# Kernel optimization log

Measured on AMD Instinct MI355X. Metric: run time of the kernel, lower is better.

Reference implementation:

```python
import jax, jax.numpy as jnp
import numpy as np

EMBED = 1024
HEADS = 16
HEAD_DIM = EMBED // HEADS
B, S = 4, 2048


def setup_inputs() -> dict:
    key = jax.random.key(0)
    ks = jax.random.split(key, 13)
    std = 1.0 / np.sqrt(EMBED)
    inp = {
        "q": jax.random.normal(ks[0], (B, S, EMBED), jnp.float32),
        "k": jax.random.normal(ks[1], (B, S, EMBED), jnp.float32),
        "v": jax.random.normal(ks[2], (B, S, EMBED), jnp.float32),
        "mask": jax.random.randint(ks[3], (B, 1, S, S), 0, 2, jnp.int32),
        "wq_w": jax.random.normal(ks[4], (EMBED, EMBED), jnp.float32) * std,
        "wq_b": jax.random.normal(ks[5], (EMBED,), jnp.float32) * std,
        "wk_w": jax.random.normal(ks[6], (EMBED, EMBED), jnp.float32) * std,
        "wk_b": jax.random.normal(ks[7], (EMBED,), jnp.float32) * std,
        "wv_w": jax.random.normal(ks[8], (EMBED, EMBED), jnp.float32) * std,
        "wv_b": jax.random.normal(ks[9], (EMBED,), jnp.float32) * std,
        "fo_w": jax.random.normal(ks[10], (EMBED, EMBED), jnp.float32) * std,
        "fo_b": jax.random.normal(ks[11], (EMBED,), jnp.float32) * std,
    }
    return inp


def reference(q, k, v, mask, wq_w, wq_b, wk_w, wk_b, wv_w, wv_b, fo_w, fo_b):
    N = q.shape[0]
    # linear projections (torch Linear: x @ W.T + b)
    qp = (q @ wq_w.T + wq_b).reshape(N, -1, HEADS, HEAD_DIM)
    kp = (k @ wk_w.T + wk_b).reshape(N, -1, HEADS, HEAD_DIM)
    vp = (v @ wv_w.T + wv_b).reshape(N, -1, HEADS, HEAD_DIM)
    # [N, H, Q, K] scores
    energy = jnp.einsum('nqhd,nkhd->nhqk', qp, kp)
    energy = jnp.where(mask == 0, jnp.float32(-1e20), energy)
    # NOTE: original scales by sqrt(embed_size), not sqrt(head_dim)
    attention = jax.nn.softmax(energy / np.float32(np.sqrt(EMBED)), axis=3)
    out = jnp.einsum('nhql,nlhd->nqhd', attention, vp).reshape(N, -1, EMBED)
    return out @ fo_w.T + fo_b
```

## Files before the change

kernel.cpp:

```cpp
#include <hip/hip_runtime.h>

typedef __attribute__((ext_vector_type(4))) float f32x4;
typedef __attribute__((ext_vector_type(16))) float f32x16;
typedef __attribute__((ext_vector_type(8))) __bf16 bf16x8;
typedef __attribute__((ext_vector_type(8))) unsigned short ushort8;
typedef __attribute__((ext_vector_type(4))) unsigned short ushort4v;
typedef __attribute__((ext_vector_type(4))) unsigned uint4v;

#define EMBED 1024
#define SEQ   2048
#define BATCH 4
#define HEADS 16
#define HDIM  64
#define SCL 0.045084220027780106f

#define GLD_LDS16(g, l) __builtin_amdgcn_global_load_lds( \
    (const __attribute__((address_space(1))) void*)(g),   \
    (__attribute__((address_space(3))) void*)(l), 16, 0, 0)
#define GLD_LDS4(g, l) __builtin_amdgcn_global_load_lds(  \
    (const __attribute__((address_space(1))) void*)(g),   \
    (__attribute__((address_space(3))) void*)(l), 4, 0, 0)

static __device__ __forceinline__ unsigned short f2bf(float f) {
  unsigned u = __builtin_bit_cast(unsigned, f);
  u += 0x7FFFu + ((u >> 16) & 1u);
  return (unsigned short)(u >> 16);
}
static __device__ __forceinline__ unsigned cvtpk(float a, float b) {
  unsigned r;
  asm("v_cvt_pk_bf16_f32 %0, %1, %2" : "=v"(r) : "v"(a), "v"(b));
  return r;
}

__global__ __launch_bounds__(256) void pack_mask_kernel(
    const int* __restrict__ m, unsigned long long* __restrict__ out) {
  int t = blockIdx.x * 256 + threadIdx.x;
  unsigned long long bits = __ballot(m[t] != 0);
  if ((threadIdx.x & 63) == 0) out[t >> 6] = bits;
}

__global__ __launch_bounds__(256) void cvt_kernel(
    const float* __restrict__ s, unsigned short* __restrict__ d, int nvec) {
  int i = blockIdx.x * 256 + threadIdx.x;
  if (i >= nvec) return;
  f32x4 a = ((const f32x4*)s)[2 * i];
  f32x4 b = ((const f32x4*)s)[2 * i + 1];
  ushort8 o;
#pragma unroll
  for (int j = 0; j < 4; ++j) { o[j] = f2bf(a[j]); o[4 + j] = f2bf(b[j]); }
  ((ushort8*)d)[i] = o;
}

__global__ __launch_bounds__(256) void cvt4_kernel(
    const float* __restrict__ s0, const float* __restrict__ s1,
    const float* __restrict__ s2, const float* __restrict__ s3,
    unsigned short* __restrict__ d, int nvec) {
  int i = blockIdx.x * 256 + threadIdx.x;
  if (i >= nvec) return;
  const float* s = (blockIdx.y == 0) ? s0 : (blockIdx.y == 1) ? s1
                 : (blockIdx.y == 2) ? s2 : s3;
  unsigned short* dd = d + (size_t)blockIdx.y * nvec * 8;
  f32x4 a = ((const f32x4*)s)[2 * i];
  f32x4 b = ((const f32x4*)s)[2 * i + 1];
  ushort8 o;
#pragma unroll
  for (int j = 0; j < 4; ++j) { o[j] = f2bf(a[j]); o[4 + j] = f2bf(b[j]); }
  ((ushort8*)dd)[i] = o;
}

template<int OUT_MODE>
__global__ __launch_bounds__(256, 3) void gemm_bt(
    const unsigned short* __restrict__ A, const unsigned short* __restrict__ B,
    const float* __restrict__ bias, void* __restrict__ outp) {
  __shared__ unsigned short Ab[3 * 128 * 32];
  __shared__ unsigned short Bb[3 * 128 * 32];
  const int tid = threadIdx.x, lane = tid & 63, wv = tid >> 6;
  const int wy = wv >> 1, wx = wv & 1, ln = lane & 15, g = lane >> 4;
  const int mbase = blockIdx.x * 128, nbase = blockIdx.y * 128;

  const int srow = tid >> 2, scol = (tid & 3) * 16;
  const char* Ag = (const char*)(A + (size_t)(mbase + srow) * EMBED) + scol;
  const char* Bg = (const char*)(B + (size_t)(nbase + srow) * EMBED) + scol;
  const size_t R64 = (size_t)64 * EMBED * 2;

  f32x4 acc[4][4];
#pragma unroll
  for (int i = 0; i < 4; i++)
#pragma unroll
    for (int j = 0; j < 4; j++) acc[i][j] = (f32x4){0.f, 0.f, 0.f, 0.f};

  auto STAGE = [&](int buf, int kt) {
    const size_t koff = (size_t)kt * 64;
    char* al = (char*)Ab + buf * 8192 + tid * 16;
    char* bl = (char*)Bb + buf * 8192 + tid * 16;
    GLD_LDS16(Ag + koff, al);
    GLD_LDS16(Ag + koff + R64, al + 4096);
    GLD_LDS16(Bg + koff, bl);
    GLD_LDS16(Bg + koff + R64, bl + 4096);
  };

  STAGE(0, 0);
  STAGE(1, 1);
  const int NT = EMBED / 32;
  int buf = 0;
  for (int kt = 0; kt < NT; ++kt) {
    __builtin_amdgcn_s_barrier();
    if (kt + 2 < NT) {
      int nb = buf + 2; if (nb >= 3) nb -= 3;
      STAGE(nb, kt + 2);
      asm volatile("s_waitcnt vmcnt(8)" ::: "memory");
    } else if (kt + 1 < NT) {
      asm volatile("s_waitcnt vmcnt(4)" ::: "memory");
    } else {
      asm volatile("s_waitcnt vmcnt(0)" ::: "memory");
    }
    __builtin_amdgcn_sched_barrier(0);
    bf16x8 af[4], bfr[4];
#pragma unroll
    for (int ms = 0; ms < 4; ++ms)
      af[ms] = __builtin_bit_cast(bf16x8,
          *(const ushort8*)&Ab[buf * 4096 + (wy * 64 + ms * 16 + ln) * 32 + g * 8]);
#pragma unroll
    for (int ns = 0; ns < 4; ++ns)
      bfr[ns] = __builtin_bit_cast(bf16x8,
          *(const ushort8*)&Bb[buf * 4096 + (wx * 64 + ns * 16 + ln) * 32 + g * 8]);
#pragma unroll
    for (int ms = 0; ms < 4; ++ms)
#pragma unroll
      for (int ns = 0; ns < 4; ++ns)
        acc[ms][ns] = __builtin_amdgcn_mfma_f32_16x16x32_bf16(
            af[ms], bfr[ns], acc[ms][ns], 0, 0, 0);
    buf = (buf == 2) ? 0 : buf + 1;
  }

  float bv[4];
#pragma unroll
  for (int ns = 0; ns < 4; ++ns) bv[ns] = bias[nbase + wx * 64 + ns * 16 + ln];

  if (OUT_MODE == 0) {
    unsigned short* out = (unsigned short*)outp;
#pragma unroll
    for (int ms = 0; ms < 4; ++ms)
#pragma unroll
      for (int ns = 0; ns < 4; ++ns) {
        int col = nbase + wx * 64 + ns * 16 + ln;
#pragma unroll
        for (int j = 0; j < 4; ++j) {
          int row = mbase + wy * 64 + ms * 16 + g * 4 + j;
          out[(size_t)row * EMBED + col] = f2bf(acc[ms][ns][j] + bv[ns]);
        }
      }
  } else if (OUT_MODE == 1) {
    unsigned short* out = (unsigned short*)outp;
#pragma unroll
    for (int ms = 0; ms < 4; ++ms)
#pragma unroll
      for (int ns = 0; ns < 4; ++ns) {
        int row0 = mbase + wy * 64 + ms * 16 + g * 4;
        int col = nbase + wx * 64 + ns * 16 + ln;
        int b = row0 >> 11, s0 = row0 & (SEQ - 1);
        int h = col >> 6, d = col & 63;
        ushort4v pk;
#pragma unroll
        for (int j = 0; j < 4; ++j) pk[j] = f2bf(acc[ms][ns][j] + bv[ns]);
        *(ushort4v*)&out[(size_t)((b * HEADS + h) * HDIM + d) * SEQ + s0] = pk;
      }
  } else {
    float* out = (float*)outp;
#pragma unroll
    for (int ms = 0; ms < 4; ++ms)
#pragma unroll
      for (int ns = 0; ns < 4; ++ns) {
        int col = nbase + wx * 64 + ns * 16 + ln;
#pragma unroll
        for (int j = 0; j < 4; ++j) {
          int row = mbase + wy * 64 + ms * 16 + g * 4 + j;
          out[(size_t)row * EMBED + col] = acc[ms][ns][j] + bv[ns];
        }
      }
  }
}

__global__ __launch_bounds__(512, 4) void attn5_kernel(
    const unsigned short* __restrict__ qp, const unsigned short* __restrict__ kp,
    const unsigned short* __restrict__ vpT,
    const unsigned long long* __restrict__ mask64,
    unsigned short* __restrict__ attb) {
  __shared__ unsigned char lds[55296];
  unsigned char* Kb = lds;
  unsigned char* Vb = lds + 24576;
  unsigned char* Mb = lds + 49152;

  const int tid = threadIdx.x;
  const int lane = tid & 63, wv = tid >> 6;
  const int lo = lane & 31, hi = lane >> 5;

  const int flat = blockIdx.x + 8 * blockIdx.y + 128 * blockIdx.z;
  const int bh = (flat & 7) * 8 + ((flat >> 3) & 7);
  const int qc = flat >> 6;
  const int b = bh >> 4, h = bh & 15;
  const int qb = qc * 256 + wv * 32;
  const int q = qb + lo;

  bf16x8 qf[4];
  {
    const unsigned short* qr = qp + (size_t)(b * SEQ + q) * EMBED + h * HDIM + hi * 8;
#pragma unroll
    for (int c = 0; c < 4; ++c) {
      ushort8 u = *(const ushort8*)(qr + 16 * c);
      bf16x8 f;
#pragma unroll
      for (int j = 0; j < 8; ++j) {
        float x = __builtin_bit_cast(float, (unsigned)u[j] << 16) * SCL;
        f[j] = (__bf16)x;
      }
      qf[c] = f;
    }
  }

  const int srow = tid >> 3;
  const int srcc = ((tid & 7) * 16) ^ (((tid >> 3) & 7) << 4);
  const char* kbase = (const char*)kp
      + ((size_t)(b * SEQ + srow) * EMBED + h * HDIM) * 2 + srcc;
  const char* vbase = (const char*)vpT
      + ((size_t)((b * HEADS + h) * HDIM + srow)) * SEQ * 2 + srcc;
  const char* mgbase = (const char*)mask64
      + ((size_t)(b * SEQ + qc * 256 + (tid >> 1)) * 32) * 8 + (tid & 1) * 4;

  auto STAGE = [&](int buf, int kt) {
    GLD_LDS16(kbase + (size_t)kt * 64 * EMBED * 2, Kb + buf * 8192 + tid * 16);
    GLD_LDS16(vbase + (size_t)kt * 128, Vb + buf * 8192 + tid * 16);
    GLD_LDS4(mgbase + kt * 8, Mb + buf * 2048 + tid * 4);
  };

  f32x16 oacc0, oacc1, oacc2;
#pragma unroll
  for (int i = 0; i < 16; ++i) { oacc0[i] = 0.f; oacc1[i] = 0.f; oacc2[i] = 0.f; }
  bf16x8 ones;
#pragma unroll
  for (int j = 0; j < 8; ++j) ones[j] = (__bf16)1.0f;

  const int swz = (lo & 7) << 4;

  STAGE(0, 0);
  STAGE(1, 1);
  const int NT = SEQ / 64;
  int buf = 0;
  for (int kt = 0; kt < NT; ++kt) {
    __builtin_amdgcn_s_barrier();
    if (kt + 2 < NT) {
      int nb = buf + 2; if (nb >= 3) nb -= 3;
      STAGE(nb, kt + 2);
      asm volatile("s_waitcnt vmcnt(6)" ::: "memory");
    } else if (kt + 1 < NT) {
      asm volatile("s_waitcnt vmcnt(3)" ::: "memory");
    } else {
      asm volatile("s_waitcnt vmcnt(0)" ::: "memory");
    }
    __builtin_amdgcn_sched_barrier(0);
    const unsigned char* Kc = Kb + buf * 8192;
    const unsigned char* Vc = Vb + buf * 8192;
    const unsigned long long mw =
        *(const unsigned long long*)(Mb + buf * 2048 + (wv * 32 + lo) * 8);

    bf16x8 PA[4];
#pragma unroll
    for (int kg = 0; kg < 2; ++kg) {
      f32x16 e;
#pragma unroll
      for (int i = 0; i < 16; ++i) e[i] = 0.f;
      const int krow = kg * 32 + lo;
#pragma unroll
      for (int c = 0; c < 4; ++c) {
        const int colb = (16 * c + 8 * hi) * 2;
        bf16x8 kf = *(const bf16x8*)(Kc + krow * 128 + (colb ^ swz));
        e = __builtin_amdgcn_mfma_f32_32x32x16_bf16(kf, qf[c], e, 0, 0, 0);
      }
      const unsigned mh = (unsigned)(mw >> (kg * 32 + 4 * hi));
      float p[16];
#pragma unroll
      for (int m = 0; m < 4; ++m)
#pragma unroll
        for (int j = 0; j < 4; ++j) {
          float pe = __builtin_amdgcn_exp2f(e[4 * m + j]);
          p[4 * m + j] = (mh & (1u << (8 * m + j))) ? pe : 0.f;
        }
      unsigned wA0 = cvtpk(p[0], p[1]),   wB0 = cvtpk(p[2], p[3]);
      unsigned wA1 = cvtpk(p[4], p[5]),   wB1 = cvtpk(p[6], p[7]);
      unsigned wA2 = cvtpk(p[8], p[9]),   wB2 = cvtpk(p[10], p[11]);
      unsigned wA3 = cvtpk(p[12], p[13]), wB3 = cvtpk(p[14], p[15]);
      asm("v_permlane32_swap_b32 %0, %1" : "+v"(wA0), "+v"(wA1));
      asm("v_permlane32_swap_b32 %0, %1" : "+v"(wB0), "+v"(wB1));
      asm("v_permlane32_swap_b32 %0, %1" : "+v"(wA2), "+v"(wA3));
      asm("v_permlane32_swap_b32 %0, %1" : "+v"(wB2), "+v"(wB3));
      PA[2 * kg]     = __builtin_bit_cast(bf16x8, (uint4v){wA0, wB0, wA1, wB1});
      PA[2 * kg + 1] = __builtin_bit_cast(bf16x8, (uint4v){wA2, wB2, wA3, wB3});
    }

    __builtin_amdgcn_s_setprio(1);
#pragma unroll
    for (int c = 0; c < 4; ++c) {
      const int pcolb = 32 * c + 16 * hi;
      bf16x8 pf = PA[c];
      {
        bf16x8 vf = *(const bf16x8*)(Vc + lo * 128 + (pcolb ^ swz));
        oacc0 = __builtin_amdgcn_mfma_f32_32x32x16_bf16(pf, vf, oacc0, 0, 0, 0);
      }
      {
        const int drow = 32 + lo;
        bf16x8 vf = *(const bf16x8*)(Vc + drow * 128 + (pcolb ^ swz));
        oacc1 = __builtin_amdgcn_mfma_f32_32x32x16_bf16(pf, vf, oacc1, 0, 0, 0);
      }
      oacc2 = __builtin_amdgcn_mfma_f32_32x32x16_bf16(pf, ones, oacc2, 0, 0, 0);
    }
    __builtin_amdgcn_s_setprio(0);
    buf = (buf == 2) ? 0 : buf + 1;
  }

#pragma unroll
  for (int r = 0; r < 16; ++r) {
    const int qq = qb + (r & 3) + 8 * (r >> 2) + 4 * hi;
    const float dinv = 1.0f / oacc2[r];
    unsigned short* orow = attb + (size_t)(b * SEQ + qq) * EMBED + h * HDIM;
    orow[lo] = f2bf(oacc0[r] * dinv);
    orow[32 + lo] = f2bf(oacc1[r] * dinv);
  }
}

extern "C" void kernel_launch(void* const* d_in, const int* in_sizes, int n_in,
                              void* d_out, int out_size, void* d_ws, size_t ws_size,
                              hipStream_t stream) {
  const float* q    = (const float*)d_in[0];
  const float* k    = (const float*)d_in[1];
  const float* v    = (const float*)d_in[2];
  const int*   mask = (const int*)d_in[3];
  const float* wq_w = (const float*)d_in[4];
  const float* wq_b = (const float*)d_in[5];
  const float* wk_w = (const float*)d_in[6];
  const float* wk_b = (const float*)d_in[7];
  const float* wv_w = (const float*)d_in[8];
  const float* wv_b = (const float*)d_in[9];
  const float* fo_w = (const float*)d_in[10];
  const float* fo_b = (const float*)d_in[11];

  char* ws = (char*)d_ws;
  const size_t MB = 1024 * 1024;
  unsigned short* stage = (unsigned short*)(ws);
  unsigned short* wqb   = (unsigned short*)(ws + 16 * MB);
  unsigned short* qp    = (unsigned short*)(ws + 24 * MB);
  unsigned short* kp    = (unsigned short*)(ws + 40 * MB);
  unsigned short* vpT   = (unsigned short*)(ws + 56 * MB);
  unsigned long long* m64 = (unsigned long long*)(ws + 72 * MB);

  const int NVX = BATCH * SEQ * EMBED / 8;
  const int NVW = EMBED * EMBED / 8;

  pack_mask_kernel<<<(BATCH * SEQ * SEQ) / 256, 256, 0, stream>>>(mask, m64);

  cvt4_kernel<<<dim3(NVW / 256, 4), 256, 0, stream>>>(wq_w, wk_w, wv_w, fo_w, wqb, NVW);
  unsigned short* wkb = wqb + (size_t)NVW * 8;
  unsigned short* wvb = wkb + (size_t)NVW * 8;
  unsigned short* fob = wvb + (size_t)NVW * 8;

  dim3 gg((BATCH * SEQ) / 128, EMBED / 128);
  cvt_kernel<<<NVX / 256, 256, 0, stream>>>(q, stage, NVX);
  gemm_bt<0><<<gg, 256, 0, stream>>>(stage, wqb, wq_b, qp);
  cvt_kernel<<<NVX / 256, 256, 0, stream>>>(k, stage, NVX);
  gemm_bt<0><<<gg, 256, 0, stream>>>(stage, wkb, wk_b, kp);
  cvt_kernel<<<NVX / 256, 256, 0, stream>>>(v, stage, NVX);
  gemm_bt<1><<<gg, 256, 0, stream>>>(stage, wvb, wv_b, vpT);

  attn5_kernel<<<dim3(8, HEADS, BATCH), 512, 0, stream>>>(qp, kp, vpT, m64, stage);

  gemm_bt<2><<<gg, 256, 0, stream>>>(stage, fob, fo_b, (float*)d_out);
}
```

Baseline: 260.8 us.

## Fuse fp32-to-bf16 activation conversion into projection GEMM loads; move waitcnt after MFMAs

After: 308.1 us. 1.18x slower.

```diff
diff --git a/kernel.cpp b/kernel.cpp
--- a/kernel.cpp
+++ b/kernel.cpp
@@ -26,6 +26,13 @@
   u += 0x7FFFu + ((u >> 16) & 1u);
   return (unsigned short)(u >> 16);
 }
+static __device__ __forceinline__ unsigned pk2bf(float a, float b) {
+  unsigned ua = __builtin_bit_cast(unsigned, a);
+  unsigned ub = __builtin_bit_cast(unsigned, b);
+  ua += 0x7FFFu + ((ua >> 16) & 1u);
+  ub += 0x7FFFu + ((ub >> 16) & 1u);
+  return (ua >> 16) | (ub & 0xFFFF0000u);
+}
 static __device__ __forceinline__ unsigned cvtpk(float a, float b) {
   unsigned r;
   asm("v_cvt_pk_bf16_f32 %0, %1, %2" : "=v"(r) : "v"(a), "v"(b));
@@ -37,18 +44,6 @@
   int t = blockIdx.x * 256 + threadIdx.x;
   unsigned long long bits = __ballot(m[t] != 0);
   if ((threadIdx.x & 63) == 0) out[t >> 6] = bits;
-}
-
-__global__ __launch_bounds__(256) void cvt_kernel(
-    const float* __restrict__ s, unsigned short* __restrict__ d, int nvec) {
-  int i = blockIdx.x * 256 + threadIdx.x;
-  if (i >= nvec) return;
-  f32x4 a = ((const f32x4*)s)[2 * i];
-  f32x4 b = ((const f32x4*)s)[2 * i + 1];
-  ushort8 o;
-#pragma unroll
-  for (int j = 0; j < 4; ++j) { o[j] = f2bf(a[j]); o[4 + j] = f2bf(b[j]); }
-  ((ushort8*)d)[i] = o;
 }
 
 __global__ __launch_bounds__(256) void cvt4_kernel(
@@ -68,20 +63,24 @@
   ((ushort8*)dd)[i] = o;
 }
 
-template<int OUT_MODE>
-__global__ __launch_bounds__(256, 3) void gemm_bt(
-    const unsigned short* __restrict__ A, const unsigned short* __restrict__ B,
+template<int OUT_MODE, bool AF32>
+__global__ __launch_bounds__(256, AF32 ? 2 : 3) void gemm_bt(
+    const void* __restrict__ Ap, const unsigned short* __restrict__ B,
     const float* __restrict__ bias, void* __restrict__ outp) {
-  __shared__ unsigned short Ab[3 * 128 * 32];
-  __shared__ unsigned short Bb[3 * 128 * 32];
+  __shared__ __attribute__((aligned(16))) char AbRaw[AF32 ? 3 * 16384 : 3 * 8192];
+  __shared__ __attribute__((aligned(16))) unsigned short Bb[3 * 128 * 32];
   const int tid = threadIdx.x, lane = tid & 63, wv = tid >> 6;
   const int wy = wv >> 1, wx = wv & 1, ln = lane & 15, g = lane >> 4;
   const int mbase = blockIdx.x * 128, nbase = blockIdx.y * 128;
 
-  const int srow = tid >> 2, scol = (tid & 3) * 16;
-  const char* Ag = (const char*)(A + (size_t)(mbase + srow) * EMBED) + scol;
-  const char* Bg = (const char*)(B + (size_t)(nbase + srow) * EMBED) + scol;
-  const size_t R64 = (size_t)64 * EMBED * 2;
+  const char* Bg = (const char*)(B + (size_t)(nbase + (tid >> 2)) * EMBED)
+                   + (tid & 3) * 16;
+  const size_t R64B = (size_t)64 * EMBED * 2;
+  const char* Agf = (const char*)Ap
+      + ((size_t)(mbase + (tid >> 3)) * EMBED) * 4
+      + (((tid & 7) * 16) ^ (((tid >> 3) & 7) << 4));
+  const char* Agb = (const char*)Ap
+      + ((size_t)(mbase + (tid >> 2)) * EMBED) * 2 + (tid & 3) * 16;
 
   f32x4 acc[4][4];
 #pragma unroll
@@ -90,36 +89,57 @@
     for (int j = 0; j < 4; j++) acc[i][j] = (f32x4){0.f, 0.f, 0.f, 0.f};
 
   auto STAGE = [&](int buf, int kt) {
-    const size_t koff = (size_t)kt * 64;
-    char* al = (char*)Ab + buf * 8192 + tid * 16;
+    if constexpr (AF32) {
+      const char* src = Agf + (size_t)kt * 128;
+      char* dst = AbRaw + buf * 16384 + tid * 16;
+#pragma unroll
+      for (int r = 0; r < 4; ++r)
+        GLD_LDS16(src + (size_t)r * 32 * EMBED * 4, dst + r * 4096);
+    } else {
+      const char* src = Agb + (size_t)kt * 64;
+      char* dst = AbRaw + buf * 8192 + tid * 16;
+      GLD_LDS16(src, dst);
+      GLD_LDS16(src + R64B, dst + 4096);
+    }
+    const char* bs = Bg + (size_t)kt * 64;
     char* bl = (char*)Bb + buf * 8192 + tid * 16;
-    GLD_LDS16(Ag + koff, al);
-    GLD_LDS16(Ag + koff + R64, al + 4096);
-    GLD_LDS16(Bg + koff, bl);
-    GLD_LDS16(Bg + koff + R64, bl + 4096);
+    GLD_LDS16(bs, bl);
+    GLD_LDS16(bs + R64B, bl + 4096);
   };
 
   STAGE(0, 0);
   STAGE(1, 1);
+  if constexpr (AF32) asm volatile("s_waitcnt vmcnt(6)" ::: "memory");
+  else                asm volatile("s_waitcnt vmcnt(4)" ::: "memory");
   const int NT = EMBED / 32;
   int buf = 0;
   for (int kt = 0; kt < NT; ++kt) {
     __builtin_amdgcn_s_barrier();
+    __builtin_amdgcn_sched_barrier(0);
     if (kt + 2 < NT) {
       int nb = buf + 2; if (nb >= 3) nb -= 3;
       STAGE(nb, kt + 2);
-      asm volatile("s_waitcnt vmcnt(8)" ::: "memory");
-    } else if (kt + 1 < NT) {
-      asm volatile("s_waitcnt vmcnt(4)" ::: "memory");
+    }
+    bf16x8 af[4], bfr[4];
+    if constexpr (AF32) {
+      const float* Af = (const float*)AbRaw + buf * 4096;
+      const int aswz = (ln & 7) << 2;
+#pragma unroll
+      for (int ms = 0; ms < 4; ++ms) {
+        const float* prow = Af + (wy * 64 + ms * 16 + ln) * 32;
+        f32x4 l4 = *(const f32x4*)(prow + ((g * 8) ^ aswz));
+        f32x4 h4 = *(const f32x4*)(prow + ((g * 8 + 4) ^ aswz));
+        af[ms] = __builtin_bit_cast(bf16x8,
+            (uint4v){pk2bf(l4[0], l4[1]), pk2bf(l4[2], l4[3]),
+                     pk2bf(h4[0], h4[1]), pk2bf(h4[2], h4[3])});
+      }
     } else {
-      asm volatile("s_waitcnt vmcnt(0)" ::: "memory");
-    }
-    __builtin_amdgcn_sched_barrier(0);
-    bf16x8 af[4], bfr[4];
-#pragma unroll
-    for (int ms = 0; ms < 4; ++ms)
-      af[ms] = __builtin_bit_cast(bf16x8,
-          *(const ushort8*)&Ab[buf * 4096 + (wy * 64 + ms * 16 + ln) * 32 + g * 8]);
+      const unsigned short* Ab = (const unsigned short*)AbRaw + buf * 4096;
+#pragma unroll
+      for (int ms = 0; ms < 4; ++ms)
+        af[ms] = __builtin_bit_cast(bf16x8,
+            *(const ushort8*)&Ab[(wy * 64 + ms * 16 + ln) * 32 + g * 8]);
+    }
 #pragma unroll
     for (int ns = 0; ns < 4; ++ns)
       bfr[ns] = __builtin_bit_cast(bf16x8,
@@ -130,6 +150,12 @@
       for (int ns = 0; ns < 4; ++ns)
         acc[ms][ns] = __builtin_amdgcn_mfma_f32_16x16x32_bf16(
             af[ms], bfr[ns], acc[ms][ns], 0, 0, 0);
+    if (kt + 2 < NT) {
+      if constexpr (AF32) asm volatile("s_waitcnt vmcnt(6)" ::: "memory");
+      else                asm volatile("s_waitcnt vmcnt(4)" ::: "memory");
+    } else if (kt + 1 < NT) {
+      asm volatile("s_waitcnt vmcnt(0)" ::: "memory");
+    }
     buf = (buf == 2) ? 0 : buf + 1;
   }
 
@@ -181,12 +207,12 @@
   }
 }
 
-__global__ __launch_bounds__(512, 4) void attn5_kernel(
+__global__ __launch_bounds__(512, 4) void attn7_kernel(
     const unsigned short* __restrict__ qp, const unsigned short* __restrict__ kp,
     const unsigned short* __restrict__ vpT,
     const unsigned long long* __restrict__ mask64,
     unsigned short* __restrict__ attb) {
-  __shared__ unsigned char lds[55296];
+  __shared__ __attribute__((aligned(16))) unsigned char lds[55296];
   unsigned char* Kb = lds;
   unsigned char* Vb = lds + 24576;
   unsigned char* Mb = lds + 49152;
@@ -244,20 +270,16 @@
 
   STAGE(0, 0);
   STAGE(1, 1);
+  asm volatile("s_waitcnt vmcnt(3)" ::: "memory");
   const int NT = SEQ / 64;
   int buf = 0;
   for (int kt = 0; kt < NT; ++kt) {
     __builtin_amdgcn_s_barrier();
+    __builtin_amdgcn_sched_barrier(0);
     if (kt + 2 < NT) {
       int nb = buf + 2; if (nb >= 3) nb -= 3;
       STAGE(nb, kt + 2);
-      asm volatile("s_waitcnt vmcnt(6)" ::: "memory");
-    } else if (kt + 1 < NT) {
-      asm volatile("s_waitcnt vmcnt(3)" ::: "memory");
-    } else {
-      asm volatile("s_waitcnt vmcnt(0)" ::: "memory");
-    }
-    __builtin_amdgcn_sched_barrier(0);
+    }
     const unsigned char* Kc = Kb + buf * 8192;
     const unsigned char* Vc = Vb + buf * 8192;
     const unsigned long long mw =
@@ -314,6 +336,11 @@
       oacc2 = __builtin_amdgcn_mfma_f32_32x32x16_bf16(pf, ones, oacc2, 0, 0, 0);
     }
     __builtin_amdgcn_s_setprio(0);
+    if (kt + 2 < NT) {
+      asm volatile("s_waitcnt vmcnt(3)" ::: "memory");
+    } else if (kt + 1 < NT) {
+      asm volatile("s_waitcnt vmcnt(0)" ::: "memory");
+    }
     buf = (buf == 2) ? 0 : buf + 1;
   }
 
@@ -352,7 +379,6 @@
   unsigned short* vpT   = (unsigned short*)(ws + 56 * MB);
   unsigned long long* m64 = (unsigned long long*)(ws + 72 * MB);
 
-  const int NVX = BATCH * SEQ * EMBED / 8;
   const int NVW = EMBED * EMBED / 8;
 
   pack_mask_kernel<<<(BATCH * SEQ * SEQ) / 256, 256, 0, stream>>>(mask, m64);
@@ -363,14 +389,11 @@
   unsigned short* fob = wvb + (size_t)NVW * 8;
 
   dim3 gg((BATCH * SEQ) / 128, EMBED / 128);
-  cvt_kernel<<<NVX / 256, 256, 0, stream>>>(q, stage, NVX);
-  gemm_bt<0><<<gg, 256, 0, stream>>>(stage, wqb, wq_b, qp);
-  cvt_kernel<<<NVX / 256, 256, 0, stream>>>(k, stage, NVX);
-  gemm_bt<0><<<gg, 256, 0, stream>>>(stage, wkb, wk_b, kp);
-  cvt_kernel<<<NVX / 256, 256, 0, stream>>>(v, stage, NVX);
-  gemm_bt<1><<<gg, 256, 0, stream>>>(stage, wvb, wv_b, vpT);
-
-  attn5_kernel<<<dim3(8, HEADS, BATCH), 512, 0, stream>>>(qp, kp, vpT, m64, stage);
-
-  gemm_bt<2><<<gg, 256, 0, stream>>>(stage, fob, fo_b, (float*)d_out);
-}
+  gemm_bt<0, true><<<gg, 256, 0, stream>>>(q, wqb, wq_b, qp);
+  gemm_bt<0, true><<<gg, 256, 0, stream>>>(k, wkb, wk_b, kp);
+  gemm_bt<1, true><<<gg, 256, 0, stream>>>(v, wvb, wv_b, vpT);
+
+  attn7_kernel<<<dim3(8, HEADS, BATCH), 512, 0, stream>>>(qp, kp, vpT, m64, stage);
+
+  gemm_bt<2, false><<<gg, 256, 0, stream>>>(stage, fob, fo_b, (float*)d_out);
+}
```
